# Kernel tuning notes

Hardware: AMD Instinct MI355X
Metric: run time of the kernel (lower is better)

The kernel has to match this reference:

```python
import jax, jax.numpy as jnp
import numpy as np

B, S, F, U = 64, 512, 128, 512          # seq_length == units (required for broadcast in original code)
SIGDIM = F + F * F                       # level-2 truncated signature dimension
GRID_SIZE, SPLINE_ORDER = 5, 3           # efficient-KAN style defaults
NB = GRID_SIZE + SPLINE_ORDER            # number of b-spline basis functions per input feature
LN_EPS = 1e-3                            # keras LayerNormalization default epsilon


def _make_grid():
    h = 2.0 / GRID_SIZE  # uniform grid on [-1, 1], extended by spline order
    return -1.0 + h * jnp.arange(-SPLINE_ORDER, GRID_SIZE + SPLINE_ORDER + 1, dtype=jnp.float32)


def _b_splines(x, grid):
    # x: (N, F) -> (N, F, NB) via Cox-de Boor recursion
    x = x[..., None]
    bases = ((x >= grid[:-1]) & (x < grid[1:])).astype(x.dtype)
    for p in range(1, SPLINE_ORDER + 1):
        left = (x - grid[:-(p + 1)]) / (grid[p:-1] - grid[:-(p + 1)])
        right = (grid[p + 1:] - x) / (grid[p + 1:] - grid[1:-p])
        bases = left * bases[..., :-1] + right * bases[..., 1:]
    return bases


def _kan_linear(x, base_w, spline_w, grid):
    # KANLinear, no bias / no layernorm: silu base branch + b-spline branch
    lead = x.shape[:-1]
    base = jax.nn.silu(x) @ base_w                                  # (..., U)
    b = _b_splines(x.reshape(-1, x.shape[-1]), grid)                # (N, F, NB)
    spl = jnp.einsum('nfk,ufk->nu', b, spline_w).reshape(*lead, base_w.shape[1])
    return base + spl


def _signature2(x):
    # level-2 path signature of piecewise-linear path x: (B, S, F) -> (B, F + F*F)
    dx = x[:, 1:] - x[:, :-1]                                       # (B, S-1, F)
    s1 = dx.sum(axis=1)                                             # (B, F)
    cs = jnp.cumsum(dx, axis=1)
    prev = jnp.concatenate([jnp.zeros_like(cs[:, :1]), cs[:, :-1]], axis=1)
    s2 = jnp.einsum('bti,btj->bij', prev + 0.5 * dx, dx)            # (B, F, F)
    return jnp.concatenate([s1, s2.reshape(x.shape[0], -1)], axis=-1)


def _grkan(sig, w1, b1, w2, b2, w3, b3, w4, b4, ws, bs, gamma, beta):
    # gated residual network mapping signature -> softmax attention weights (B, U)
    h = jax.nn.elu(sig @ w1 + b1)
    h = h @ w2 + b2
    glu = jax.nn.sigmoid(h @ w3 + b3) * (h @ w4 + b4)
    y = sig @ ws + bs + glu
    mu = jnp.mean(y, axis=-1, keepdims=True)
    var = jnp.var(y, axis=-1, keepdims=True)
    y = (y - mu) / jnp.sqrt(var + LN_EPS) * gamma + beta
    return jax.nn.softmax(y, axis=-1)


def setup_inputs() -> dict:
    key = jax.random.key(0)
    ks = jax.random.split(key, 24)
    n = lambda k, shp, s=0.02: jax.random.normal(k, shp, dtype=jnp.float32) * s
    inp = {
        'inputs': jax.random.normal(ks[0], (B, S, F), dtype=jnp.float32),
        'h_prev': jax.random.normal(ks[1], (B, U), dtype=jnp.float32),
        'c_prev': jax.random.normal(ks[2], (B, U), dtype=jnp.float32),
        'time_kernel': n(ks[3], (S, 1), 0.1),
        'kan_base_w': n(ks[4], (F, U)),
        'kan_spline_w': n(ks[5], (U, F, NB)),
        'g_w1': n(ks[6], (SIGDIM, U)), 'g_b1': jnp.zeros((U,), jnp.float32),
        'g_w2': n(ks[7], (U, U)), 'g_b2': jnp.zeros((U,), jnp.float32),
        'g_w3': n(ks[8], (U, U)), 'g_b3': jnp.zeros((U,), jnp.float32),
        'g_w4': n(ks[9], (U, U)), 'g_b4': jnp.zeros((U,), jnp.float32),
        'g_skip_w': n(ks[10], (SIGDIM, U)), 'g_skip_b': jnp.zeros((U,), jnp.float32),
        'ln_gamma': jnp.ones((U,), jnp.float32), 'ln_beta': jnp.zeros((U,), jnp.float32),
        'wf': n(ks[11], (2 * U, U)), 'bf': jnp.zeros((U,), jnp.float32),
        'wi': n(ks[12], (2 * U, U)), 'bi': jnp.zeros((U,), jnp.float32),
        'wc': n(ks[13], (2 * U, U)), 'bc': jnp.zeros((U,), jnp.float32),
        'wo': n(ks[14], (2 * U, U)), 'bo': jnp.zeros((U,), jnp.float32),
    }
    return inp


def reference(inputs, h_prev, c_prev, time_kernel, kan_base_w, kan_spline_w,
              g_w1, g_b1, g_w2, g_b2, g_w3, g_b3, g_w4, g_b4, g_skip_w, g_skip_b,
              ln_gamma, ln_beta, wf, bf, wi, bi, wc, bc, wo, bo):
    grid = _make_grid()
    weighted = time_kernel * inputs                                  # (B,S,F)
    sig = _signature2(weighted)                                      # (B,SIGDIM)
    attn = _grkan(sig, g_w1, g_b1, g_w2, g_b2, g_w3, g_b3, g_w4, g_b4,
                  g_skip_w, g_skip_b, ln_gamma, ln_beta)             # (B,S) since U==S
    kan_out = _kan_linear(weighted, kan_base_w, kan_spline_w, grid)  # (B,S,U)
    attended = kan_out * attn[..., None]                             # (B,S,U)
    current = attended.mean(axis=1)                                  # (B,U)
    combined = jnp.concatenate([current, h_prev], axis=-1)           # (B,2U)
    f = jax.nn.sigmoid(combined @ wf + bf)
    i = jax.nn.sigmoid(combined @ wi + bi)
    cand = jnp.tanh(combined @ wc + bc)
    o = jax.nn.sigmoid(combined @ wo + bo)
    c_new = f * c_prev + i * cand
    h_new = o * jnp.tanh(c_new)
    return h_new, c_new
```

## Files before the change

kernel.cpp:

```cpp
#include <hip/hip_runtime.h>
#include <math.h>

#define BB 64
#define SS 512
#define FF 128
#define UU 512
#define NBB 8
#define SIGDIM (FF + FF*FF)
#define K3 16512
#define KK 1152

typedef __attribute__((ext_vector_type(8))) __bf16 bf16x8;
typedef __attribute__((ext_vector_type(8))) unsigned short u16x8;
typedef __attribute__((ext_vector_type(4))) float f32x4;

__device__ __forceinline__ unsigned short f2bf(float x) {
    unsigned int u = __float_as_uint(x);
    unsigned int r = u + 0x7FFFu + ((u >> 16) & 1u);
    return (unsigned short)(r >> 16);
}

__device__ __forceinline__ float sigmoidf(float x) { return 1.0f / (1.0f + expf(-x)); }

__global__ void k_wprep(const float* __restrict__ splw, const float* __restrict__ basew,
                        const float* __restrict__ h_prev,
                        unsigned short* __restrict__ Wt, unsigned short* __restrict__ comb_b) {
    int idx = blockIdx.x * 256 + threadIdx.x;
    if (idx >= UU * KK) return;
    int u = idx / KK, c = idx % KK;
    float v = (c < 1024) ? splw[(size_t)u * 1024 + c] : basew[(size_t)(c - 1024) * UU + u];
    Wt[idx] = f2bf(v);
    if (idx < BB * UU) {
        int b = idx >> 9, uu = idx & 511;
        comb_b[(size_t)b * 1024 + 512 + uu] = f2bf(h_prev[idx]);
    }
}

__global__ __launch_bounds__(256) void k_wt3(const float* __restrict__ w2, const float* __restrict__ w3,
                                             const float* __restrict__ w4, const float* __restrict__ wf,
                                             const float* __restrict__ wi, const float* __restrict__ wc,
                                             const float* __restrict__ wo,
                                             unsigned short* __restrict__ W2t,
                                             unsigned short* __restrict__ W3t,
                                             unsigned short* __restrict__ W4t,
                                             unsigned short* __restrict__ Wgt) {
    int kt = blockIdx.x, ut = blockIdx.y, z = blockIdx.z;
    int Kdim = (z < 3) ? 512 : 1024;
    if (kt * 64 >= Kdim) return;
    const float* src;
    unsigned short* dst;
    switch (z) {
        case 0: src = w2; dst = W2t; break;
        case 1: src = w3; dst = W3t; break;
        case 2: src = w4; dst = W4t; break;
        case 3: src = wf; dst = Wgt; break;
        case 4: src = wi; dst = Wgt + (size_t)512 * 1024; break;
        case 5: src = wc; dst = Wgt + (size_t)1024 * 1024; break;
        default: src = wo; dst = Wgt + (size_t)1536 * 1024; break;
    }
    __shared__ float tile[64][67];
    int tid = threadIdx.x;
    int k0 = kt * 64, u0 = ut * 64;
#pragma unroll
    for (int p = 0; p < 4; ++p) {
        int e = p * 256 + tid;
        int kk = e >> 4, c4 = (e & 15) * 4;
        const float4 v = *(const float4*)(src + (size_t)(k0 + kk) * UU + u0 + c4);
        tile[kk][c4 + 0] = v.x;
        tile[kk][c4 + 1] = v.y;
        tile[kk][c4 + 2] = v.z;
        tile[kk][c4 + 3] = v.w;
    }
    __syncthreads();
    int kk0 = (tid & 7) * 8;
#pragma unroll
    for (int p = 0; p < 2; ++p) {
        int uu = (tid >> 3) + p * 32;
        u16x8 ov;
#pragma unroll
        for (int j = 0; j < 8; ++j) ov[j] = f2bf(tile[kk0 + j][uu]);
        *(u16x8*)(dst + (size_t)(u0 + uu) * Kdim + k0 + kk0) = ov;
    }
}

__global__ __launch_bounds__(256) void k_wt2(const float* __restrict__ w1,
                                             const float* __restrict__ gsw,
                                             unsigned short* __restrict__ W1t,
                                             unsigned short* __restrict__ Wst) {
    int kt = blockIdx.x, ut = blockIdx.y, mat = blockIdx.z;
    const float* src = mat ? gsw : w1;
    unsigned short* dst = mat ? Wst : W1t;
    __shared__ float tile[64][67];
    int tid = threadIdx.x;
    int k0 = kt * 64, u0 = ut * 64;
#pragma unroll
    for (int p = 0; p < 4; ++p) {
        int e = p * 256 + tid;
        int kk = e >> 4, c4 = (e & 15) * 4;
        const float4 v = *(const float4*)(src + (size_t)(k0 + kk) * UU + u0 + c4);
        tile[kk][c4 + 0] = v.x;
        tile[kk][c4 + 1] = v.y;
        tile[kk][c4 + 2] = v.z;
        tile[kk][c4 + 3] = v.w;
    }
    __syncthreads();
    int kk0 = (tid & 7) * 8;
#pragma unroll
    for (int p = 0; p < 2; ++p) {
        int uu = (tid >> 3) + p * 32;
        u16x8 ov;
#pragma unroll
        for (int j = 0; j < 8; ++j) ov[j] = f2bf(tile[kk0 + j][uu]);
        *(u16x8*)(dst + (size_t)(u0 + uu) * K3 + k0 + kk0) = ov;
    }
}

__global__ __launch_bounds__(256) void k_adprep(const float* __restrict__ inp,
                                                const float* __restrict__ tk,
                                                unsigned short* __restrict__ aT,
                                                unsigned short* __restrict__ dT,
                                                unsigned short* __restrict__ wT) {
    int tt0 = blockIdx.x * 64, f0 = blockIdx.y * 64, b = blockIdx.z;
    __shared__ float wS[65][67];
    __shared__ float w0S[64];
    int tid = threadIdx.x;
    const float* ib = inp + (size_t)b * SS * FF;
    if (tid < 64) w0S[tid] = tk[0] * ib[f0 + tid];
#pragma unroll
    for (int p = 0; p < 5; ++p) {
        int e = p * 256 + tid;
        if (e < 65 * 16) {
            int row = e >> 4, c4 = (e & 15) * 4;
            int t = tt0 + row;
            if (t < SS) {
                float tkt = tk[t];
                const float4 v = *(const float4*)(ib + (size_t)t * FF + f0 + c4);
                wS[row][c4 + 0] = tkt * v.x;
                wS[row][c4 + 1] = tkt * v.y;
                wS[row][c4 + 2] = tkt * v.z;
                wS[row][c4 + 3] = tkt * v.w;
            } else {
                wS[row][c4 + 0] = 0.f;
                wS[row][c4 + 1] = 0.f;
                wS[row][c4 + 2] = 0.f;
                wS[row][c4 + 3] = 0.f;
            }
        }
    }
    __syncthreads();
    int t8 = (tid & 7) * 8;
#pragma unroll
    for (int p = 0; p < 2; ++p) {
        int ff = (tid >> 3) + p * 32;
        float w0 = w0S[ff];
        u16x8 av, dv, wv;
#pragma unroll
        for (int j = 0; j < 8; ++j) {
            int tt = t8 + j;
            float w = wS[tt][ff];
            float wn = wS[tt + 1][ff];
            bool valid = (tt0 + tt) < (SS - 1);
            float a = valid ? 0.5f * (w + wn) - w0 : 0.f;
            float d = valid ? wn - w : 0.f;
            av[j] = f2bf(a);
            dv[j] = f2bf(d);
            wv[j] = f2bf(w);
        }
        size_t o = ((size_t)b * FF + f0 + ff) * SS + tt0 + t8;
        *(u16x8*)(aT + o) = av;
        *(u16x8*)(dT + o) = dv;
        *(u16x8*)(wT + o) = wv;
    }
}

__global__ __launch_bounds__(256) void k_sig_mfma(const unsigned short* __restrict__ aT,
                                                  const unsigned short* __restrict__ dT,
                                                  float* __restrict__ s2part) {
    int kc = blockIdx.x, b = blockIdx.y;
    int tid = threadIdx.x, lane = tid & 63;
    int wv = __builtin_amdgcn_readfirstlane(tid >> 6);
    int wrow = (wv & 1) * 64, wcol = (wv >> 1) * 64;
    int k0 = kc * 128;
    const unsigned short* pa = aT + ((size_t)b * FF + wrow + (lane & 15)) * SS + k0 + (lane >> 4) * 8;
    const unsigned short* pd = dT + ((size_t)b * FF + wcol + (lane & 15)) * SS + k0 + (lane >> 4) * 8;
    f32x4 acc[4][4];
#pragma unroll
    for (int i = 0; i < 4; ++i)
#pragma unroll
        for (int j = 0; j < 4; ++j) acc[i][j] = (f32x4)(0.f);
#pragma unroll
    for (int t = 0; t < 4; ++t) {
        bf16x8 af[4], df[4];
#pragma unroll
        for (int rt = 0; rt < 4; ++rt) af[rt] = *(const bf16x8*)(pa + (size_t)rt * 16 * SS + t * 32);
#pragma unroll
        for (int ct = 0; ct < 4; ++ct) df[ct] = *(const bf16x8*)(pd + (size_t)ct * 16 * SS + t * 32);
#pragma unroll
        for (int rt = 0; rt < 4; ++rt)
#pragma unroll
            for (int ct = 0; ct < 4; ++ct)
                acc[rt][ct] = __builtin_amdgcn_mfma_f32_16x16x32_bf16(af[rt], df[ct], acc[rt][ct], 0, 0, 0);
    }
    float* outp = s2part + ((size_t)kc * BB + b) * (FF * FF);
    int quad = lane >> 4, col = lane & 15;
#pragma unroll
    for (int rt = 0; rt < 4; ++rt)
#pragma unroll
        for (int ct = 0; ct < 4; ++ct)
#pragma unroll
            for (int reg = 0; reg < 4; ++reg)
                outp[(wrow + rt * 16 + quad * 4 + reg) * FF + wcol + ct * 16 + col] = acc[rt][ct][reg];
}

__global__ void k_sig_reduce(const float* __restrict__ inp, const float* __restrict__ tk,
                             const float* __restrict__ s2part, unsigned short* __restrict__ sigb) {
    int idx = blockIdx.x * 256 + threadIdx.x;
    if (idx >= BB * SIGDIM) return;
    int b = idx / SIGDIM, r = idx % SIGDIM;
    float v;
    if (r < FF) {
        v = tk[SS - 1] * inp[((size_t)b * SS + SS - 1) * FF + r] - tk[0] * inp[(size_t)b * SS * FF + r];
    } else {
        int ij = r - FF;
        v = 0.f;
#pragma unroll
        for (int c = 0; c < 4; ++c) v += s2part[((size_t)c * BB + b) * (FF * FF) + ij];
    }
    sigb[idx] = f2bf(v);
}

__global__ __launch_bounds__(64) void k_sig_direct(const unsigned short* __restrict__ sigb,
                                                   const unsigned short* __restrict__ W1t,
                                                   const unsigned short* __restrict__ Wst,
                                                   const float* __restrict__ b1,
                                                   unsigned short* __restrict__ h1b,
                                                   float* __restrict__ skippre) {
    int lane = threadIdx.x;
    int mt = blockIdx.x, nt = blockIdx.y, mat = blockIdx.z;
    const unsigned short* Bp = mat ? Wst : W1t;
    const unsigned short* pa = sigb + (size_t)(mt * 16 + (lane & 15)) * K3 + (lane >> 4) * 8;
    const unsigned short* pb = Bp + (size_t)(nt * 16 + (lane & 15)) * K3 + (lane >> 4) * 8;
    f32x4 acc0 = (f32x4)(0.f), acc1 = (f32x4)(0.f);
#pragma unroll 8
    for (int t = 0; t < K3 / 32; t += 2) {
        bf16x8 a0 = *(const bf16x8*)(pa + t * 32);
        bf16x8 b0 = *(const bf16x8*)(pb + t * 32);
        bf16x8 a1 = *(const bf16x8*)(pa + t * 32 + 32);
        bf16x8 b1v = *(const bf16x8*)(pb + t * 32 + 32);
        acc0 = __builtin_amdgcn_mfma_f32_16x16x32_bf16(a0, b0, acc0, 0, 0, 0);
        acc1 = __builtin_amdgcn_mfma_f32_16x16x32_bf16(a1, b1v, acc1, 0, 0, 0);
    }
    int col = lane & 15, quad = lane >> 4;
    int j = nt * 16 + col;
    if (mat == 0) {
        float bb = b1[j];
#pragma unroll
        for (int reg = 0; reg < 4; ++reg) {
            int row = mt * 16 + quad * 4 + reg;
            float v = acc0[reg] + acc1[reg] + bb;
            h1b[(size_t)row * UU + j] = f2bf(v > 0.f ? v : expf(v) - 1.0f);
        }
    } else {
#pragma unroll
        for (int reg = 0; reg < 4; ++reg) {
            int row = mt * 16 + quad * 4 + reg;
            skippre[(size_t)row * UU + j] = acc0[reg] + acc1[reg];
        }
    }
}

__global__ __launch_bounds__(64) void k_h2_direct(const unsigned short* __restrict__ h1b,
                                                  const unsigned short* __restrict__ W2t,
                                                  const float* __restrict__ b2,
                                                  unsigned short* __restrict__ h2b) {
    int lane = threadIdx.x;
    int mt = blockIdx.x, nt = blockIdx.y;
    const unsigned short* pa = h1b + (size_t)(mt * 16 + (lane & 15)) * 512 + (lane >> 4) * 8;
    const unsigned short* pb = W2t + (size_t)(nt * 16 + (lane & 15)) * 512 + (lane >> 4) * 8;
    f32x4 acc0 = (f32x4)(0.f), acc1 = (f32x4)(0.f);
#pragma unroll
    for (int t = 0; t < 16; t += 2) {
        bf16x8 a0 = *(const bf16x8*)(pa + t * 32);
        bf16x8 b0 = *(const bf16x8*)(pb + t * 32);
        bf16x8 a1 = *(const bf16x8*)(pa + t * 32 + 32);
        bf16x8 b1v = *(const bf16x8*)(pb + t * 32 + 32);
        acc0 = __builtin_amdgcn_mfma_f32_16x16x32_bf16(a0, b0, acc0, 0, 0, 0);
        acc1 = __builtin_amdgcn_mfma_f32_16x16x32_bf16(a1, b1v, acc1, 0, 0, 0);
    }
    int col = lane & 15, quad = lane >> 4;
    int j = nt * 16 + col;
    float bb = b2[j];
#pragma unroll
    for (int reg = 0; reg < 4; ++reg) {
        int row = mt * 16 + quad * 4 + reg;
        h2b[(size_t)row * UU + j] = f2bf(acc0[reg] + acc1[reg] + bb);
    }
}

__global__ __launch_bounds__(64) void k_glu_direct(const unsigned short* __restrict__ h2b,
                                                   const unsigned short* __restrict__ W3t,
                                                   const unsigned short* __restrict__ W4t,
                                                   const float* __restrict__ b3,
                                                   const float* __restrict__ b4,
                                                   const float* __restrict__ skippre,
                                                   const float* __restrict__ skb,
                                                   float* __restrict__ yv) {
    int lane = threadIdx.x;
    int mt = blockIdx.x, nt = blockIdx.y;
    const unsigned short* pa = h2b + (size_t)(mt * 16 + (lane & 15)) * 512 + (lane >> 4) * 8;
    const unsigned short* pb3 = W3t + (size_t)(nt * 16 + (lane & 15)) * 512 + (lane >> 4) * 8;
    const unsigned short* pb4 = W4t + (size_t)(nt * 16 + (lane & 15)) * 512 + (lane >> 4) * 8;
    f32x4 acc3 = (f32x4)(0.f), acc4 = (f32x4)(0.f);
#pragma unroll
    for (int t = 0; t < 16; ++t) {
        bf16x8 a = *(const bf16x8*)(pa + t * 32);
        bf16x8 b3f = *(const bf16x8*)(pb3 + t * 32);
        bf16x8 b4f = *(const bf16x8*)(pb4 + t * 32);
        acc3 = __builtin_amdgcn_mfma_f32_16x16x32_bf16(a, b3f, acc3, 0, 0, 0);
        acc4 = __builtin_amdgcn_mfma_f32_16x16x32_bf16(a, b4f, acc4, 0, 0, 0);
    }
    int col = lane & 15, quad = lane >> 4;
    int j = nt * 16 + col;
    float bb3 = b3[j], bb4 = b4[j], sb = skb[j];
#pragma unroll
    for (int reg = 0; reg < 4; ++reg) {
        int row = mt * 16 + quad * 4 + reg;
        float g = sigmoidf(acc3[reg] + bb3);
        yv[(size_t)row * UU + j] = skippre[(size_t)row * UU + j] + sb + g * (acc4[reg] + bb4);
    }
}

__device__ __forceinline__ float block_sum(float v, float* red) {
    int tid = threadIdx.x;
#pragma unroll
    for (int off = 32; off > 0; off >>= 1) v += __shfl_down(v, off);
    __syncthreads();
    if ((tid & 63) == 0) red[tid >> 6] = v;
    __syncthreads();
    float r = red[0];
#pragma unroll
    for (int i = 1; i < 8; ++i) r += red[i];
    return r;
}
__device__ __forceinline__ float block_max(float v, float* red) {
    int tid = threadIdx.x;
#pragma unroll
    for (int off = 32; off > 0; off >>= 1) v = fmaxf(v, __shfl_down(v, off));
    __syncthreads();
    if ((tid & 63) == 0) red[tid >> 6] = v;
    __syncthreads();
    float r = red[0];
#pragma unroll
    for (int i = 1; i < 8; ++i) r = fmaxf(r, red[i]);
    return r;
}

__global__ void k_lnsm(const float* __restrict__ yv, const float* __restrict__ gamma,
                       const float* __restrict__ beta, float* __restrict__ attn) {
    int b = blockIdx.x, u = threadIdx.x;
    __shared__ float red[8];
    float v = yv[(size_t)b * UU + u];
    float mu = block_sum(v, red) * (1.0f / UU);
    float d = v - mu;
    float var = block_sum(d * d, red) * (1.0f / UU);
    float z = d * rsqrtf(var + 1e-3f) * gamma[u] + beta[u];
    float m = block_max(z, red);
    float e = expf(z - m);
    float Z = block_sum(e, red);
    attn[(size_t)b * UU + u] = e / Z;
}

__global__ __launch_bounds__(256) void k_kan_red(const unsigned short* __restrict__ wT,
                                                 const float* __restrict__ attn,
                                                 unsigned short* __restrict__ Aredb) {
    int b = blockIdx.x;
    int lane = threadIdx.x & 63;
    int f = blockIdx.y * 4 + (threadIdx.x >> 6);

    const u16x8 wv = *(const u16x8*)(wT + ((size_t)b * FF + f) * SS + lane * 8);
    const float* ap = attn + (size_t)b * UU + lane * 8;
    float4 a0 = *(const float4*)ap;
    float4 a1 = *(const float4*)(ap + 4);

    float acc[9] = {};
#pragma unroll
    for (int s = 0; s < 8; ++s) {
        float w = __uint_as_float((unsigned int)wv[s] << 16);
        float a = (s < 4) ? ((s == 0) ? a0.x : (s == 1) ? a0.y : (s == 2) ? a0.z : a0.w)
                          : ((s == 4) ? a1.x : (s == 5) ? a1.y : (s == 6) ? a1.z : a1.w);
        float t = (w + 2.2f) * 2.5f;
        float cf = floorf(fminf(fmaxf(t, -2.f), 13.f));
        int c = (int)cf;
        float u = t - cf;
        float u2 = u * u, u3 = u2 * u;
        float p0 = u3 * (1.f / 6.f);
        float p1 = (-3.f * u3 + 3.f * u2 + 3.f * u + 1.f) * (1.f / 6.f);
        float p2 = (3.f * u3 - 6.f * u2 + 4.f) * (1.f / 6.f);
        float onemu = 1.f - u;
        float p3 = onemu * onemu * onemu * (1.f / 6.f);
#pragma unroll
        for (int k2 = 0; k2 < 8; ++k2) {
            int d = c - k2;
            float v = (d == 0) ? p0 : (d == 1) ? p1 : (d == 2) ? p2 : (d == 3) ? p3 : 0.f;
            acc[k2] += a * v;
        }
        acc[8] += a * (w * sigmoidf(w));
    }

#pragma unroll
    for (int off = 1; off < 64; off <<= 1) {
#pragma unroll
        for (int k = 0; k < 9; ++k) acc[k] += __shfl_xor(acc[k], off);
    }

    if (lane == 0) {
        const float sc = 1.0f / SS;
        u16x8 ov;
#pragma unroll
        for (int k = 0; k < 8; ++k) ov[k] = f2bf(acc[k] * sc);
        *(u16x8*)(Aredb + (size_t)b * KK + f * 8) = ov;
        Aredb[(size_t)b * KK + 1024 + f] = f2bf(acc[8] * sc);
    }
}

__global__ __launch_bounds__(64) void k_cur_direct(const unsigned short* __restrict__ Aredb,
                                                   const unsigned short* __restrict__ Wt,
                                                   unsigned short* __restrict__ comb_b) {
    int lane = threadIdx.x;
    int mt = blockIdx.x, nt = blockIdx.y;
    const unsigned short* pa = Aredb + (size_t)(mt * 16 + (lane & 15)) * KK + (lane >> 4) * 8;
    const unsigned short* pb = Wt + (size_t)(nt * 16 + (lane & 15)) * KK + (lane >> 4) * 8;
    f32x4 acc0 = (f32x4)(0.f), acc1 = (f32x4)(0.f);
#pragma unroll 6
    for (int t = 0; t < KK / 32; t += 2) {
        bf16x8 a0 = *(const bf16x8*)(pa + t * 32);
        bf16x8 b0 = *(const bf16x8*)(pb + t * 32);
        bf16x8 a1 = *(const bf16x8*)(pa + t * 32 + 32);
        bf16x8 b1v = *(const bf16x8*)(pb + t * 32 + 32);
        acc0 = __builtin_amdgcn_mfma_f32_16x16x32_bf16(a0, b0, acc0, 0, 0, 0);
        acc1 = __builtin_amdgcn_mfma_f32_16x16x32_bf16(a1, b1v, acc1, 0, 0, 0);
    }
    int col = lane & 15, quad = lane >> 4;
    int j = nt * 16 + col;
#pragma unroll
    for (int reg = 0; reg < 4; ++reg) {
        int row = mt * 16 + quad * 4 + reg;
        comb_b[(size_t)row * 1024 + j] = f2bf(acc0[reg] + acc1[reg]);
    }
}

__global__ __launch_bounds__(64) void k_gates_direct(const unsigned short* __restrict__ comb_b,
                                                     const unsigned short* __restrict__ Wgt,
                                                     float* __restrict__ gates) {
    int lane = threadIdx.x;
    int mt = blockIdx.x, nt = blockIdx.y;
    const unsigned short* pa = comb_b + (size_t)(mt * 16 + (lane & 15)) * 1024 + (lane >> 4) * 8;
    const unsigned short* pb = Wgt + (size_t)(nt * 16 + (lane & 15)) * 1024 + (lane >> 4) * 8;
    f32x4 acc0 = (f32x4)(0.f), acc1 = (f32x4)(0.f);
#pragma unroll 8
    for (int t = 0; t < 32; t += 2) {
        bf16x8 a0 = *(const bf16x8*)(pa + t * 32);
        bf16x8 b0 = *(const bf16x8*)(pb + t * 32);
        bf16x8 a1 = *(const bf16x8*)(pa + t * 32 + 32);
        bf16x8 b1v = *(const bf16x8*)(pb + t * 32 + 32);
        acc0 = __builtin_amdgcn_mfma_f32_16x16x32_bf16(a0, b0, acc0, 0, 0, 0);
        acc1 = __builtin_amdgcn_mfma_f32_16x16x32_bf16(a1, b1v, acc1, 0, 0, 0);
    }
    int col = lane & 15, quad = lane >> 4;
    int j = nt * 16 + col;
#pragma unroll
    for (int reg = 0; reg < 4; ++reg) {
        int row = mt * 16 + quad * 4 + reg;
        gates[(size_t)row * 2048 + j] = acc0[reg] + acc1[reg];
    }
}

__global__ void k_cell(const float* __restrict__ gates,
                       const float* __restrict__ bf_, const float* __restrict__ bi_,
                       const float* __restrict__ bc_, const float* __restrict__ bo_,
                       const float* __restrict__ c_prev, float* __restrict__ out) {
    int idx = blockIdx.x * 256 + threadIdx.x;
    if (idx >= BB * UU) return;
    int b = idx >> 9, u = idx & 511;
    const float* g = gates + (size_t)b * 2048;
    float f = sigmoidf(g[u] + bf_[u]);
    float ii = sigmoidf(g[512 + u] + bi_[u]);
    float cd = tanhf(g[1024 + u] + bc_[u]);
    float o = sigmoidf(g[1536 + u] + bo_[u]);
    float cn = f * c_prev[idx] + ii * cd;
    out[idx] = o * tanhf(cn);
    out[(size_t)BB * UU + idx] = cn;
}

extern "C" void kernel_launch(void* const* d_in, const int* in_sizes, int n_in,
                              void* d_out, int out_size, void* d_ws, size_t ws_size,
                              hipStream_t stream) {
    const float* inp   = (const float*)d_in[0];
    const float* hprev = (const float*)d_in[1];
    const float* cprev = (const float*)d_in[2];
    const float* tk    = (const float*)d_in[3];
    const float* basew = (const float*)d_in[4];
    const float* splw  = (const float*)d_in[5];
    const float* gw1   = (const float*)d_in[6];
    const float* gb1   = (const float*)d_in[7];
    const float* gw2   = (const float*)d_in[8];
    const float* gb2   = (const float*)d_in[9];
    const float* gw3   = (const float*)d_in[10];
    const float* gb3   = (const float*)d_in[11];
    const float* gw4   = (const float*)d_in[12];
    const float* gb4   = (const float*)d_in[13];
    const float* gsw   = (const float*)d_in[14];
    const float* gsb   = (const float*)d_in[15];
    const float* lng   = (const float*)d_in[16];
    const float* lnb   = (const float*)d_in[17];
    const float* wf    = (const float*)d_in[18];
    const float* bf_   = (const float*)d_in[19];
    const float* wi    = (const float*)d_in[20];
    const float* bi_   = (const float*)d_in[21];
    const float* wc    = (const float*)d_in[22];
    const float* bc_   = (const float*)d_in[23];
    const float* wo    = (const float*)d_in[24];
    const float* bo_   = (const float*)d_in[25];
    float* out = (float*)d_out;

    float* ws = (float*)d_ws;
    size_t o = 0;
    unsigned short* W1t = (unsigned short*)(ws + o); o += (size_t)UU * K3 / 2;
    unsigned short* Wst = (unsigned short*)(ws + o); o += (size_t)UU * K3 / 2;
    unsigned short* Wt  = (unsigned short*)(ws + o); o += (size_t)UU * KK / 2;
    float* s2part   = ws + o; o += (size_t)4 * BB * FF * FF;
    unsigned short* aT = (unsigned short*)(ws + o); o += (size_t)BB * FF * SS / 2;
    unsigned short* dT = (unsigned short*)(ws + o); o += (size_t)BB * FF * SS / 2;
    unsigned short* wT = (unsigned short*)(ws + o); o += (size_t)BB * FF * SS / 2;
    unsigned short* sigb = (unsigned short*)(ws + o); o += (size_t)BB * K3 / 2;
    float* skippre  = ws + o; o += (size_t)BB * UU;
    unsigned short* h1b = (unsigned short*)(ws + o); o += (size_t)BB * UU / 2;
    unsigned short* h2b = (unsigned short*)(ws + o); o += (size_t)BB * UU / 2;
    float* yv       = ws + o; o += (size_t)BB * UU;
    float* attn     = ws + o; o += (size_t)BB * UU;
    unsigned short* Aredb = (unsigned short*)(ws + o); o += (size_t)BB * KK / 2;
    unsigned short* W2t = (unsigned short*)(ws + o); o += (size_t)512 * 512 / 2;
    unsigned short* W3t = (unsigned short*)(ws + o); o += (size_t)512 * 512 / 2;
    unsigned short* W4t = (unsigned short*)(ws + o); o += (size_t)512 * 512 / 2;
    unsigned short* Wgt = (unsigned short*)(ws + o); o += (size_t)2048 * 1024 / 2;
    unsigned short* comb_b = (unsigned short*)(ws + o); o += (size_t)BB * 1024 / 2;
    float* gates    = ws + o; o += (size_t)BB * 2048;
    (void)ws_size; (void)in_sizes; (void)n_in; (void)out_size;

    k_wprep<<<(UU * KK + 255) / 256, 256, 0, stream>>>(splw, basew, hprev, Wt, comb_b);
    k_wt3<<<dim3(16, 8, 7), 256, 0, stream>>>(gw2, gw3, gw4, wf, wi, wc, wo, W2t, W3t, W4t, Wgt);
    k_wt2<<<dim3(K3 / 64, UU / 64, 2), 256, 0, stream>>>(gw1, gsw, W1t, Wst);
    k_adprep<<<dim3(8, 2, BB), 256, 0, stream>>>(inp, tk, aT, dT, wT);
    k_sig_mfma<<<dim3(4, BB), 256, 0, stream>>>(aT, dT, s2part);
    k_sig_reduce<<<(BB * SIGDIM + 255) / 256, 256, 0, stream>>>(inp, tk, s2part, sigb);
    k_sig_direct<<<dim3(4, 32, 2), 64, 0, stream>>>(sigb, W1t, Wst, gb1, h1b, skippre);
    k_h2_direct<<<dim3(4, 32), 64, 0, stream>>>(h1b, W2t, gb2, h2b);
    k_glu_direct<<<dim3(4, 32), 64, 0, stream>>>(h2b, W3t, W4t, gb3, gb4, skippre, gsb, yv);
    k_lnsm<<<BB, UU, 0, stream>>>(yv, lng, lnb, attn);
    k_kan_red<<<dim3(BB, FF / 4), 256, 0, stream>>>(wT, attn, Aredb);
    k_cur_direct<<<dim3(4, 32), 64, 0, stream>>>(Aredb, Wt, comb_b);
    k_gates_direct<<<dim3(4, 128), 64, 0, stream>>>(comb_b, Wgt, gates);
    k_cell<<<(BB * UU + 255) / 256, 256, 0, stream>>>(gates, bf_, bi_, bc_, bo_, cprev, out);
}
```

Measured before the change: 273.9 us.

## Fuse W1/skip weight bf16 transpose into split-K signature GEMM

Removes the separate pass that transposed and converted the large fp32 W1 and skip weights (16512x512 each) to bf16. The new kernel reads the fp32 weights directly, converts them to bf16 in shared memory per K-tile, and runs MFMA against the signature with a split-K grid of 43 chunks. A second kernel sums the partials and applies the bias and ELU. This avoids writing and re-reading the bf16 weight copies and raises parallelism over the old 256-wave GEMM, at the cost of an extra partial-sum buffer and a reduction pass.

```diff
diff --git a/kernel.cpp b/kernel.cpp
--- a/kernel.cpp
+++ b/kernel.cpp
@@ -9,6 +9,8 @@
 #define SIGDIM (FF + FF*FF)
 #define K3 16512
 #define KK 1152
+#define SIG_KC 43
+#define SIG_STEPS 6
 
 typedef __attribute__((ext_vector_type(8))) __bf16 bf16x8;
 typedef __attribute__((ext_vector_type(8))) unsigned short u16x8;
@@ -83,38 +85,6 @@
     }
 }
 
-__global__ __launch_bounds__(256) void k_wt2(const float* __restrict__ w1,
-                                             const float* __restrict__ gsw,
-                                             unsigned short* __restrict__ W1t,
-                                             unsigned short* __restrict__ Wst) {
-    int kt = blockIdx.x, ut = blockIdx.y, mat = blockIdx.z;
-    const float* src = mat ? gsw : w1;
-    unsigned short* dst = mat ? Wst : W1t;
-    __shared__ float tile[64][67];
-    int tid = threadIdx.x;
-    int k0 = kt * 64, u0 = ut * 64;
-#pragma unroll
-    for (int p = 0; p < 4; ++p) {
-        int e = p * 256 + tid;
-        int kk = e >> 4, c4 = (e & 15) * 4;
-        const float4 v = *(const float4*)(src + (size_t)(k0 + kk) * UU + u0 + c4);
-        tile[kk][c4 + 0] = v.x;
-        tile[kk][c4 + 1] = v.y;
-        tile[kk][c4 + 2] = v.z;
-        tile[kk][c4 + 3] = v.w;
-    }
-    __syncthreads();
-    int kk0 = (tid & 7) * 8;
-#pragma unroll
-    for (int p = 0; p < 2; ++p) {
-        int uu = (tid >> 3) + p * 32;
-        u16x8 ov;
-#pragma unroll
-        for (int j = 0; j < 8; ++j) ov[j] = f2bf(tile[kk0 + j][uu]);
-        *(u16x8*)(dst + (size_t)(u0 + uu) * K3 + k0 + kk0) = ov;
-    }
-}
-
 __global__ __launch_bounds__(256) void k_adprep(const float* __restrict__ inp,
                                                 const float* __restrict__ tk,
                                                 unsigned short* __restrict__ aT,
@@ -229,43 +199,82 @@
     sigb[idx] = f2bf(v);
 }
 
-__global__ __launch_bounds__(64) void k_sig_direct(const unsigned short* __restrict__ sigb,
-                                                   const unsigned short* __restrict__ W1t,
-                                                   const unsigned short* __restrict__ Wst,
-                                                   const float* __restrict__ b1,
-                                                   unsigned short* __restrict__ h1b,
-                                                   float* __restrict__ skippre) {
-    int lane = threadIdx.x;
-    int mt = blockIdx.x, nt = blockIdx.y, mat = blockIdx.z;
-    const unsigned short* Bp = mat ? Wst : W1t;
-    const unsigned short* pa = sigb + (size_t)(mt * 16 + (lane & 15)) * K3 + (lane >> 4) * 8;
-    const unsigned short* pb = Bp + (size_t)(nt * 16 + (lane & 15)) * K3 + (lane >> 4) * 8;
-    f32x4 acc0 = (f32x4)(0.f), acc1 = (f32x4)(0.f);
-#pragma unroll 8
-    for (int t = 0; t < K3 / 32; t += 2) {
-        bf16x8 a0 = *(const bf16x8*)(pa + t * 32);
-        bf16x8 b0 = *(const bf16x8*)(pb + t * 32);
-        bf16x8 a1 = *(const bf16x8*)(pa + t * 32 + 32);
-        bf16x8 b1v = *(const bf16x8*)(pb + t * 32 + 32);
-        acc0 = __builtin_amdgcn_mfma_f32_16x16x32_bf16(a0, b0, acc0, 0, 0, 0);
-        acc1 = __builtin_amdgcn_mfma_f32_16x16x32_bf16(a1, b1v, acc1, 0, 0, 0);
-    }
+__global__ __launch_bounds__(256) void k_sig_fused(const unsigned short* __restrict__ sigb,
+                                                   const float* __restrict__ w1,
+                                                   const float* __restrict__ gsw,
+                                                   float* __restrict__ spart) {
+    int nt = blockIdx.x, kc = blockIdx.y, mat = blockIdx.z;
+    const float* src = mat ? gsw : w1;
+    __shared__ float tile[64][67];
+    int tid = threadIdx.x, lane = tid & 63;
+    int wv = __builtin_amdgcn_readfirstlane(tid >> 6);
+    int u0 = nt * 64;
+    int n0 = wv * 16;
+    int kbase = kc * (SIG_STEPS * 64);
+
+    f32x4 acc[4];
+#pragma unroll
+    for (int i = 0; i < 4; ++i) acc[i] = (f32x4)(0.f);
+
+    int nn = lane & 15;
+    int kq = (lane >> 4) * 8;
+    const unsigned short* pab = sigb + (size_t)nn * K3 + kq;
+
+    for (int step = 0; step < SIG_STEPS; ++step) {
+        int k0 = kbase + step * 64;
+#pragma unroll
+        for (int p = 0; p < 4; ++p) {
+            int e = p * 256 + tid;
+            int kk = e >> 4, c4 = (e & 15) * 4;
+            const float4 v = *(const float4*)(src + (size_t)(k0 + kk) * UU + u0 + c4);
+            tile[kk][c4 + 0] = v.x;
+            tile[kk][c4 + 1] = v.y;
+            tile[kk][c4 + 2] = v.z;
+            tile[kk][c4 + 3] = v.w;
+        }
+        __syncthreads();
+#pragma unroll
+        for (int s = 0; s < 2; ++s) {
+            u16x8 ub;
+            int kb = s * 32 + kq;
+#pragma unroll
+            for (int j = 0; j < 8; ++j) ub[j] = f2bf(tile[kb + j][n0 + nn]);
+            bf16x8 bfrag = __builtin_bit_cast(bf16x8, ub);
+#pragma unroll
+            for (int rt = 0; rt < 4; ++rt) {
+                bf16x8 afrag = *(const bf16x8*)(pab + (size_t)(rt * 16) * K3 + k0 + s * 32);
+                acc[rt] = __builtin_amdgcn_mfma_f32_16x16x32_bf16(afrag, bfrag, acc[rt], 0, 0, 0);
+            }
+        }
+        __syncthreads();
+    }
+
     int col = lane & 15, quad = lane >> 4;
-    int j = nt * 16 + col;
+    float* P = spart + ((size_t)(mat * SIG_KC + kc) * 64) * UU;
+#pragma unroll
+    for (int rt = 0; rt < 4; ++rt)
+#pragma unroll
+        for (int reg = 0; reg < 4; ++reg)
+            P[(size_t)(rt * 16 + quad * 4 + reg) * UU + u0 + n0 + col] = acc[rt][reg];
+}
+
+__global__ __launch_bounds__(256) void k_sig_red2(const float* __restrict__ spart,
+                                                  const float* __restrict__ b1,
+                                                  unsigned short* __restrict__ h1b,
+                                                  float* __restrict__ skippre) {
+    int idx = blockIdx.x * 256 + threadIdx.x;
+    int mat = idx >> 15;
+    int rem = idx & 32767;
+    int m = rem >> 9, n = rem & 511;
+    const float* p = spart + ((size_t)(mat * SIG_KC) * 64 + m) * UU + n;
+    float v = 0.f;
+#pragma unroll
+    for (int kc = 0; kc < SIG_KC; ++kc) v += p[(size_t)kc * 64 * UU];
     if (mat == 0) {
-        float bb = b1[j];
-#pragma unroll
-        for (int reg = 0; reg < 4; ++reg) {
-            int row = mt * 16 + quad * 4 + reg;
-            float v = acc0[reg] + acc1[reg] + bb;
-            h1b[(size_t)row * UU + j] = f2bf(v > 0.f ? v : expf(v) - 1.0f);
-        }
+        v += b1[n];
+        h1b[(size_t)m * UU + n] = f2bf(v > 0.f ? v : expf(v) - 1.0f);
     } else {
-#pragma unroll
-        for (int reg = 0; reg < 4; ++reg) {
-            int row = mt * 16 + quad * 4 + reg;
-            skippre[(size_t)row * UU + j] = acc0[reg] + acc1[reg];
-        }
+        skippre[(size_t)m * UU + n] = v;
     }
 }
 
@@ -525,14 +534,13 @@
 
     float* ws = (float*)d_ws;
     size_t o = 0;
-    unsigned short* W1t = (unsigned short*)(ws + o); o += (size_t)UU * K3 / 2;
-    unsigned short* Wst = (unsigned short*)(ws + o); o += (size_t)UU * K3 / 2;
     unsigned short* Wt  = (unsigned short*)(ws + o); o += (size_t)UU * KK / 2;
     float* s2part   = ws + o; o += (size_t)4 * BB * FF * FF;
     unsigned short* aT = (unsigned short*)(ws + o); o += (size_t)BB * FF * SS / 2;
     unsigned short* dT = (unsigned short*)(ws + o); o += (size_t)BB * FF * SS / 2;
     unsigned short* wT = (unsigned short*)(ws + o); o += (size_t)BB * FF * SS / 2;
     unsigned short* sigb = (unsigned short*)(ws + o); o += (size_t)BB * K3 / 2;
+    float* spart    = ws + o; o += (size_t)2 * SIG_KC * 64 * UU;
     float* skippre  = ws + o; o += (size_t)BB * UU;
     unsigned short* h1b = (unsigned short*)(ws + o); o += (size_t)BB * UU / 2;
     unsigned short* h2b = (unsigned short*)(ws + o); o += (size_t)BB * UU / 2;
@@ -549,11 +557,11 @@
 
     k_wprep<<<(UU * KK + 255) / 256, 256, 0, stream>>>(splw, basew, hprev, Wt, comb_b);
     k_wt3<<<dim3(16, 8, 7), 256, 0, stream>>>(gw2, gw3, gw4, wf, wi, wc, wo, W2t, W3t, W4t, Wgt);
-    k_wt2<<<dim3(K3 / 64, UU / 64, 2), 256, 0, stream>>>(gw1, gsw, W1t, Wst);
     k_adprep<<<dim3(8, 2, BB), 256, 0, stream>>>(inp, tk, aT, dT, wT);
     k_sig_mfma<<<dim3(4, BB), 256, 0, stream>>>(aT, dT, s2part);
     k_sig_reduce<<<(BB * SIGDIM + 255) / 256, 256, 0, stream>>>(inp, tk, s2part, sigb);
-    k_sig_direct<<<dim3(4, 32, 2), 64, 0, stream>>>(sigb, W1t, Wst, gb1, h1b, skippre);
+    k_sig_fused<<<dim3(8, SIG_KC, 2), 256, 0, stream>>>(sigb, gw1, gsw, spart);
+    k_sig_red2<<<256, 256, 0, stream>>>(spart, gb1, h1b, skippre);
     k_h2_direct<<<dim3(4, 32), 64, 0, stream>>>(h1b, W2t, gb2, h2b);
     k_glu_direct<<<dim3(4, 32), 64, 0, stream>>>(h2b, W3t, W4t, gb3, gb4, skippre, gsb, yv);
     k_lnsm<<<BB, UU, 0, stream>>>(yv, lng, lnb, attn);
```

After: 252.1 us. 1.09x faster.
